# Performance work log

Hardware: AMD Instinct MI355X
Metric: run time of the kernel (lower is better)

The kernel has to match this reference:

```python
import jax, jax.numpy as jnp
import numpy as np

# Sinabs LIF semantics (norm_input=True default):
#   v[t] = alpha * v[t-1] + (1 - alpha) * x[t],  alpha = exp(-1/tau_mem)
#   spikes = MultiSpike: max(floor(v / threshold), 0)   (default sa.ActivationFunction)
#   reset  = MembraneSubtract: v -= spikes * threshold
# threshold_low=None -> no lower clamp.

TAU_MEM = 20.0
THRESHOLD = 1.0
GRAD_WIDTH = 0.5   # sinabs SingleExponential surrogate defaults
GRAD_SCALE = 1.0

@jax.custom_vjp
def spike_fn(v):
    # MultiSpike: number of threshold crossings this step
    return jnp.maximum(jnp.floor(v / THRESHOLD), 0.0)

def _spike_fwd(v):
    return spike_fn(v), v

def _spike_bwd(v, g):
    # single-exponential surrogate gradient around threshold
    sg = (GRAD_SCALE / GRAD_WIDTH) * jnp.exp(-jnp.abs(v - THRESHOLD) / GRAD_WIDTH)
    return (g * sg,)

spike_fn.defvjp(_spike_fwd, _spike_bwd)

def lif_layer(x):
    # x: [B, T, N] synaptic input; returns spikes [B, T, N]
    alpha = jnp.exp(jnp.asarray(-1.0 / TAU_MEM, dtype=x.dtype))
    one_m = 1.0 - alpha

    def step(v, xt):
        v = alpha * v + one_m * xt
        s = spike_fn(v)
        v = v - s * THRESHOLD  # membrane subtract reset
        return v, s

    v0 = jnp.zeros(x.shape[:1] + x.shape[2:], dtype=x.dtype)  # [B, N]
    _, spikes = jax.lax.scan(step, v0, jnp.swapaxes(x, 0, 1))  # scan over T
    return jnp.swapaxes(spikes, 0, 1)

def setup_inputs() -> dict:
    key = jax.random.key(0)
    k0, k1, k2, k3 = jax.random.split(key, 4)
    B, T, C_IN = 256, 4096, 16
    data = jax.random.normal(k0, (B, T, C_IN), dtype=jnp.float32)
    # nn.Linear(in, out, bias=False) weights are [out, in], kaiming-uniform-ish scale
    w1 = jax.random.normal(k1, (16, 16), dtype=jnp.float32) / np.sqrt(16)
    w2 = jax.random.normal(k2, (32, 16), dtype=jnp.float32) / np.sqrt(16)
    w3 = jax.random.normal(k3, (10, 32), dtype=jnp.float32) / np.sqrt(32)
    return {"data": data, "w1": w1, "w2": w2, "w3": w3}

def reference(data, w1, w2, w3):
    out = jnp.einsum('btc,oc->bto', data, w1)
    out = lif_layer(out)
    out = jnp.einsum('btc,oc->bto', out, w2)
    out = lif_layer(out)
    out = jnp.einsum('btc,oc->bto', out, w3)
    out = lif_layer(out)
    return out
```

## Files before the change

### kernel.cpp

```cpp
#include <hip/hip_runtime.h>
#include <stdint.h>
#include <math.h>

#define T_STEPS 4096
#define BATCH   256
#define NB_BLK  256
#define NSEG    1024
#define EPITCH  1025

__device__ __forceinline__ float lif_step(float& v, float xs, float alpha) {
    float vp = fmaf(alpha, v, xs);
    float fr = vp - floorf(vp);
    float vn = fminf(vp, fr);
    float s  = vp - vn;
    v = vn;
    return s;
}

__device__ __forceinline__ float ubf(uint32_t w, int k) {
    return (float)((w >> (k * 8)) & 0xffu);
}

__device__ __forceinline__ float sgpr_f(float v) {
    return __uint_as_float(__builtin_amdgcn_readfirstlane(__float_as_uint(v)));
}

__device__ __forceinline__ float dot16(const float wr[16],
    float4 c0, float4 c1, float4 c2, float4 c3)
{
    float p0 = fmaf(wr[1], c0.y, wr[0] * c0.x);
    p0 = fmaf(wr[2], c0.z, p0);  p0 = fmaf(wr[3], c0.w, p0);
    float p1 = fmaf(wr[5], c1.y, wr[4] * c1.x);
    p1 = fmaf(wr[6], c1.z, p1);  p1 = fmaf(wr[7], c1.w, p1);
    float p2 = fmaf(wr[9], c2.y, wr[8] * c2.x);
    p2 = fmaf(wr[10], c2.z, p2); p2 = fmaf(wr[11], c2.w, p2);
    float p3 = fmaf(wr[13], c3.y, wr[12] * c3.x);
    p3 = fmaf(wr[14], c3.z, p3); p3 = fmaf(wr[15], c3.w, p3);
    return (p0 + p1) + (p2 + p3);
}

__global__ __launch_bounds__(1024) void fused(
    const float* __restrict__ x, const float* __restrict__ w1,
    const float* __restrict__ w2, const float* __restrict__ w3,
    float* __restrict__ out, uint8_t* __restrict__ s1t,
    uint8_t* __restrict__ s2t,
    float alpha, float one_m, float alpha4)
{
    const int tid = threadIdx.x;
    const int b   = blockIdx.x;
    const int wv  = tid >> 6;
    const int ln  = tid & 63;

    __shared__ float2   sh_cert[16][EPITCH];
    __shared__ uint32_t sh_badseg[16][NSEG / 32];
    __shared__ uint8_t  sh_bm1[NB_BLK];
    __shared__ uint8_t  sh_bm2[NB_BLK];
    __shared__ int      sh_badch, sh_spike, sh_flag2;

    const float* xb = x + (size_t)b * T_STEPS * 16;
    const float4* xq4 = (const float4*)xb;

    if (tid < 64)        ((uint32_t*)sh_bm1)[tid] = 0u;
    else if (tid < 128)  ((uint32_t*)sh_bm2)[tid - 64] = 0u;
    else if (tid == 128) { sh_badch = 0; sh_spike = 0; sh_flag2 = 0; }

    float4* o4 = (float4*)(out + (size_t)b * T_STEPS * 10);
    float4 z4 = make_float4(0.f, 0.f, 0.f, 0.f);
#pragma unroll
    for (int i = 0; i < 10; ++i) o4[i * 1024 + tid] = z4;

    const float alpha2 = alpha * alpha;

    {
        float4 xr[8];
#pragma unroll
        for (int q = 0; q < 8; ++q) xr[q] = xq4[tid * 16 + q];
#pragma unroll 2
        for (int c = 0; c < 16; ++c) {
            float wc[16];
#pragma unroll
            for (int i = 0; i < 16; ++i) wc[i] = sgpr_f(w1[c * 16 + i]);
            float y0 = dot16(wc, xr[0], xr[1], xr[2], xr[3]);
            float y1 = dot16(wc, xr[4], xr[5], xr[6], xr[7]);
            float a0 = one_m * y0;
            float a1 = fmaf(alpha, a0, one_m * y1);
            sh_cert[c][tid] = make_float2(a1, fmaxf(a0, a1));
        }
    }
    {
        float4 xr[8];
#pragma unroll
        for (int q = 0; q < 8; ++q) xr[q] = xq4[tid * 16 + 8 + q];
#pragma unroll 2
        for (int c = 0; c < 16; ++c) {
            float wc[16];
#pragma unroll
            for (int i = 0; i < 16; ++i) wc[i] = sgpr_f(w1[c * 16 + i]);
            float y2 = dot16(wc, xr[0], xr[1], xr[2], xr[3]);
            float y3 = dot16(wc, xr[4], xr[5], xr[6], xr[7]);
            float b0 = one_m * y2;
            float b1 = fmaf(alpha, b0, one_m * y3);
            float mB = fmaxf(b0, b1);
            float2 ca = sh_cert[c][tid];
            float end = fmaf(alpha2, ca.x, b1);
            float m0  = fmaxf(ca.y, fmaf(alpha, fmaxf(ca.x, 0.0f), mB));
            sh_cert[c][tid] = make_float2(end, m0);
        }
    }
    __syncthreads();

    if (tid < 128) {
        const int c  = tid & 15;
        const int e8 = tid >> 4;
        const int s0 = e8 * 128;
        float vs = 0.0f;
        if (e8 > 0) {
#pragma unroll 8
            for (int s = s0 - 40; s < s0; ++s)
                vs = fmaf(alpha4, vs, sh_cert[c][s].x);
        }
        uint32_t bw = 0;
        int bad = 0;
#pragma unroll 8
        for (int s = s0; s < s0 + 128; ++s) {
            float2 ct = sh_cert[c][s];
            float vsu = fminf(fmaxf(vs + 1e-3f, 0.0f), 1.0f);
            float bound = fmaf(alpha, vsu, ct.y);
            if (!(bound < 0.999f)) { bw |= 1u << (s & 31); bad = 1; }
            if ((s & 31) == 31) { sh_badseg[c][s >> 5] = bw; bw = 0; }
            vs = fmaf(alpha4, vs, ct.x);
        }
        if (bad) atomicOr(&sh_badch, 1 << c);
    }
    __syncthreads();

    const int badmask = sh_badch;
    if (badmask) {
        uint4* sz = (uint4*)(s1t + (size_t)b * 16 * T_STEPS);
#pragma unroll
        for (int i = 0; i < 4; ++i) sz[i * 1024 + tid] = make_uint4(0u,0u,0u,0u);
        __syncthreads();

        int m = badmask;
        for (int i = 0; i < wv; ++i) m &= m - 1;
        if (ln == 0 && m) {
            const int c = __ffs(m) - 1;
            float wc[16];
#pragma unroll
            for (int i = 0; i < 16; ++i) wc[i] = w1[c * 16 + i];
            uint8_t* op = s1t + ((size_t)b * 16 + c) * T_STEPS;
            float v = 0.0f;
            int any = 0;
            for (int w32 = 0; w32 < 32; ++w32) {
                uint32_t bwv = sh_badseg[c][w32];
                const int sb = w32 * 32;
                if (bwv == 0u) {
#pragma unroll 8
                    for (int q = 0; q < 32; ++q)
                        v = fmaf(alpha4, v, sh_cert[c][sb + q].x);
                } else {
                    for (int q = 0; q < 32; ++q) {
                        const int s = sb + q;
                        if (!((bwv >> q) & 1u)) {
                            v = fmaf(alpha4, v, sh_cert[c][s].x);
                            continue;
                        }
                        const float4* xr2 = xq4 + (size_t)s * 16;
                        uint32_t sw = 0u;
#pragma unroll
                        for (int j = 0; j < 4; ++j) {
                            float y = dot16(wc, xr2[j*4+0], xr2[j*4+1],
                                                 xr2[j*4+2], xr2[j*4+3]);
                            float sp = lif_step(v, one_m * y, alpha);
                            sw |= ((uint32_t)(int)sp) << (j * 8);
                        }
                        if (sw) {
                            *(uint32_t*)(op + s * 4) = sw;
                            sh_bm1[s >> 2] = 1;
                            any = 1;
                        }
                    }
                }
            }
            if (any) sh_spike = 1;
        }
    }
    __syncthreads();

    if (sh_spike) {
        if (tid < 32) {
            const int c2 = tid;
            float wr2[16];
#pragma unroll
            for (int i = 0; i < 16; ++i) wr2[i] = one_m * w2[c2 * 16 + i];
            const uint8_t* sb1 = s1t + (size_t)b * 16 * T_STEPS;
            uint4* op2 = (uint4*)(s2t + ((size_t)b * 32 + c2) * T_STEPS);
            const uint4* bmv = (const uint4*)sh_bm1;
            float v = 0.0f;
            for (int sb = 0; sb < 16; ++sb) {
                uint4 bm = bmv[sb];
                if ((bm.x | bm.y | bm.z | bm.w) == 0u) {
                    if (v != 0.0f) {
                        for (int blk = 0; blk < 16 && v != 0.0f; ++blk) {
#pragma unroll
                            for (int j = 0; j < 16; ++j) v *= alpha;
                        }
                    }
                    continue;
                }
                for (int blk = 0; blk < 16; ++blk) {
                    uint32_t d = (blk < 4) ? bm.x : (blk < 8) ? bm.y
                               : (blk < 12) ? bm.z : bm.w;
                    uint32_t byte = (d >> ((blk & 3) * 8)) & 0xffu;
                    if (byte == 0u) {
                        if (v != 0.0f) {
#pragma unroll
                            for (int j = 0; j < 16; ++j) v *= alpha;
                        }
                        continue;
                    }
                    const int tb = sb * 16 + blk;
                    const int t0 = tb * 16;
                    uint4 S[16];
#pragma unroll
                    for (int c = 0; c < 16; ++c)
                        S[c] = *(const uint4*)(sb1 + (size_t)c * T_STEPS + t0);
                    uint32_t w[4] = {0u, 0u, 0u, 0u};
#pragma unroll
                    for (int j = 0; j < 16; ++j) {
                        float xv[16];
#pragma unroll
                        for (int c = 0; c < 16; ++c) {
                            uint32_t dd = (j < 4) ? S[c].x : (j < 8) ? S[c].y
                                        : (j < 12) ? S[c].z : S[c].w;
                            xv[c] = ubf(dd, j & 3);
                        }
                        float p0 = fmaf(wr2[1], xv[1], wr2[0] * xv[0]);
                        p0 = fmaf(wr2[2], xv[2], p0);   p0 = fmaf(wr2[3], xv[3], p0);
                        float p1 = fmaf(wr2[5], xv[5], wr2[4] * xv[4]);
                        p1 = fmaf(wr2[6], xv[6], p1);   p1 = fmaf(wr2[7], xv[7], p1);
                        float p2 = fmaf(wr2[9], xv[9], wr2[8] * xv[8]);
                        p2 = fmaf(wr2[10], xv[10], p2); p2 = fmaf(wr2[11], xv[11], p2);
                        float p3 = fmaf(wr2[13], xv[13], wr2[12] * xv[12]);
                        p3 = fmaf(wr2[14], xv[14], p3); p3 = fmaf(wr2[15], xv[15], p3);
                        float xs = (p0 + p1) + (p2 + p3);
                        float s = lif_step(v, xs, alpha);
                        w[j >> 2] |= ((uint32_t)(int)s) << ((j & 3) * 8);
                    }
                    op2[tb] = make_uint4(w[0], w[1], w[2], w[3]);
                    if (w[0] | w[1] | w[2] | w[3]) { sh_bm2[tb] = 1; sh_flag2 = 1; }
                }
            }
        }
        __syncthreads();

        if (sh_flag2 && tid < 16) {
            const int c3 = tid;
            const bool active = (c3 < 10);
            float wr3[32];
#pragma unroll
            for (int i = 0; i < 32; ++i)
                wr3[i] = active ? (one_m * w3[c3 * 32 + i]) : 0.0f;
            const uint8_t* sb2 = s2t + (size_t)b * 32 * T_STEPS;
            const uint4* bmv2 = (const uint4*)sh_bm2;
            float* ob = out + (size_t)b * T_STEPS * 10 + c3;
            float v = 0.0f;
            for (int sb = 0; sb < 16; ++sb) {
                uint4 bm = bmv2[sb];
                if ((bm.x | bm.y | bm.z | bm.w) == 0u) {
                    if (v != 0.0f) {
                        for (int blk = 0; blk < 16 && v != 0.0f; ++blk) {
#pragma unroll
                            for (int j = 0; j < 16; ++j) v *= alpha;
                        }
                    }
                    continue;
                }
                for (int blk = 0; blk < 16; ++blk) {
                    uint32_t d = (blk < 4) ? bm.x : (blk < 8) ? bm.y
                               : (blk < 12) ? bm.z : bm.w;
                    uint32_t byte = (d >> ((blk & 3) * 8)) & 0xffu;
                    if (byte == 0u) {
                        if (v != 0.0f) {
#pragma unroll
                            for (int j = 0; j < 16; ++j) v *= alpha;
                        }
                        continue;
                    }
                    const int t0 = (sb * 16 + blk) * 16;
                    uint4 S[32];
#pragma unroll
                    for (int c = 0; c < 32; ++c)
                        S[c] = *(const uint4*)(sb2 + (size_t)c * T_STEPS + t0);
#pragma unroll
                    for (int j = 0; j < 16; ++j) {
                        float xv[32];
#pragma unroll
                        for (int c = 0; c < 32; ++c) {
                            uint32_t dd = (j < 4) ? S[c].x : (j < 8) ? S[c].y
                                        : (j < 12) ? S[c].z : S[c].w;
                            xv[c] = ubf(dd, j & 3);
                        }
                        float p0 = fmaf(wr3[1], xv[1], wr3[0] * xv[0]);
                        p0 = fmaf(wr3[2],  xv[2],  p0); p0 = fmaf(wr3[3],  xv[3],  p0);
                        p0 = fmaf(wr3[4],  xv[4],  p0); p0 = fmaf(wr3[5],  xv[5],  p0);
                        p0 = fmaf(wr3[6],  xv[6],  p0); p0 = fmaf(wr3[7],  xv[7],  p0);
                        float p1 = fmaf(wr3[9], xv[9], wr3[8] * xv[8]);
                        p1 = fmaf(wr3[10], xv[10], p1); p1 = fmaf(wr3[11], xv[11], p1);
                        p1 = fmaf(wr3[12], xv[12], p1); p1 = fmaf(wr3[13], xv[13], p1);
                        p1 = fmaf(wr3[14], xv[14], p1); p1 = fmaf(wr3[15], xv[15], p1);
                        float p2 = fmaf(wr3[17], xv[17], wr3[16] * xv[16]);
                        p2 = fmaf(wr3[18], xv[18], p2); p2 = fmaf(wr3[19], xv[19], p2);
                        p2 = fmaf(wr3[20], xv[20], p2); p2 = fmaf(wr3[21], xv[21], p2);
                        p2 = fmaf(wr3[22], xv[22], p2); p2 = fmaf(wr3[23], xv[23], p2);
                        float p3 = fmaf(wr3[25], xv[25], wr3[24] * xv[24]);
                        p3 = fmaf(wr3[26], xv[26], p3); p3 = fmaf(wr3[27], xv[27], p3);
                        p3 = fmaf(wr3[28], xv[28], p3); p3 = fmaf(wr3[29], xv[29], p3);
                        p3 = fmaf(wr3[30], xv[30], p3); p3 = fmaf(wr3[31], xv[31], p3);
                        float xs = (p0 + p1) + (p2 + p3);
                        float s = lif_step(v, xs, alpha);
                        if (active && s != 0.0f) ob[(size_t)(t0 + j) * 10] = s;
                    }
                }
            }
        }
    }
}

extern "C" void kernel_launch(void* const* d_in, const int* in_sizes, int n_in,
                              void* d_out, int out_size, void* d_ws, size_t ws_size,
                              hipStream_t stream)
{
    const float* data = (const float*)d_in[0];
    const float* w1   = (const float*)d_in[1];
    const float* w2   = (const float*)d_in[2];
    const float* w3   = (const float*)d_in[3];
    float* out = (float*)d_out;

    uint8_t* ws  = (uint8_t*)d_ws;
    uint8_t* s1t = ws;
    uint8_t* s2t = ws + (16u << 20);

    const float alpha  = expf(-1.0f / 20.0f);
    const float one_m  = 1.0f - alpha;
    const float alpha4 = expf(-4.0f / 20.0f);

    fused<<<BATCH, 1024, 0, stream>>>(data, w1, w2, w3, out, s1t, s2t,
                                      alpha, one_m, alpha4);
}
```

Baseline: 150.1 us.

## Split fused LIF kernel into channel-half layer-1 blocks and separate tail kernel

Layer 1 now runs as 512-thread blocks, two per batch row, each handling 8 of the 16 channels. Per-segment bound data is stored as float ends plus 16-bit quantized maxima, and the certificate bound is tightened with a second maximum term. Layers 2 and 3 move into a separate 64-thread kernel that reads a global block bitmap and flags, and a memset is added to clear them. The goal is higher occupancy and less shared memory per block. The cost is an extra launch, a memset, and global round-trips for the bitmaps.

```diff
diff --git a/kernel.cpp b/kernel.cpp
--- a/kernel.cpp
+++ b/kernel.cpp
@@ -4,9 +4,8 @@
 
 #define T_STEPS 4096
 #define BATCH   256
-#define NB_BLK  256
 #define NSEG    1024
-#define EPITCH  1025
+#define CPITCH  9
 
 __device__ __forceinline__ float lif_step(float& v, float xs, float alpha) {
     float vp = fmaf(alpha, v, xs);
@@ -23,6 +22,15 @@
 
 __device__ __forceinline__ float sgpr_f(float v) {
     return __uint_as_float(__builtin_amdgcn_readfirstlane(__float_as_uint(v)));
+}
+
+__device__ __forceinline__ unsigned short encq(float m) {
+    int q = (int)ceilf(fmaf(m, 4096.0f, 32768.0f));
+    q = q < 0 ? 0 : (q > 65534 ? 65535 : q);
+    return (unsigned short)q;
+}
+__device__ __forceinline__ float decq(unsigned short q) {
+    return (q == 65535) ? 1e30f : fmaf((float)q, 0.000244140625f, -8.0f);
 }
 
 __device__ __forceinline__ float dot16(const float wr[16],
@@ -39,96 +47,110 @@
     return (p0 + p1) + (p2 + p3);
 }
 
-__global__ __launch_bounds__(1024) void fused(
+__global__ __launch_bounds__(512) void lif1(
     const float* __restrict__ x, const float* __restrict__ w1,
-    const float* __restrict__ w2, const float* __restrict__ w3,
     float* __restrict__ out, uint8_t* __restrict__ s1t,
-    uint8_t* __restrict__ s2t,
+    uint8_t* __restrict__ bm1, int* __restrict__ flag1,
     float alpha, float one_m, float alpha4)
 {
     const int tid = threadIdx.x;
-    const int b   = blockIdx.x;
+    const int bh  = blockIdx.x;
+    const int b   = bh >> 1;
+    const int cg  = bh & 1;
     const int wv  = tid >> 6;
     const int ln  = tid & 63;
 
-    __shared__ float2   sh_cert[16][EPITCH];
-    __shared__ uint32_t sh_badseg[16][NSEG / 32];
-    __shared__ uint8_t  sh_bm1[NB_BLK];
-    __shared__ uint8_t  sh_bm2[NB_BLK];
-    __shared__ int      sh_badch, sh_spike, sh_flag2;
-
-    const float* xb = x + (size_t)b * T_STEPS * 16;
-    const float4* xq4 = (const float4*)xb;
-
-    if (tid < 64)        ((uint32_t*)sh_bm1)[tid] = 0u;
-    else if (tid < 128)  ((uint32_t*)sh_bm2)[tid - 64] = 0u;
-    else if (tid == 128) { sh_badch = 0; sh_spike = 0; sh_flag2 = 0; }
+    __shared__ float          endf[NSEG * CPITCH];
+    __shared__ unsigned short m0q [NSEG * CPITCH];
+    __shared__ unsigned short m1q [NSEG * CPITCH];
+    __shared__ uint32_t       sh_badseg[8][32];
+    __shared__ int            sh_badch;
+
+    const float4* xq4 = (const float4*)(x + (size_t)b * T_STEPS * 16);
+
+    if (tid == 0) sh_badch = 0;
 
     float4* o4 = (float4*)(out + (size_t)b * T_STEPS * 10);
     float4 z4 = make_float4(0.f, 0.f, 0.f, 0.f);
 #pragma unroll
-    for (int i = 0; i < 10; ++i) o4[i * 1024 + tid] = z4;
-
-    const float alpha2 = alpha * alpha;
-
-    {
-        float4 xr[8];
-#pragma unroll
-        for (int q = 0; q < 8; ++q) xr[q] = xq4[tid * 16 + q];
+    for (int i = 0; i < 10; ++i) o4[cg * 5120 + i * 512 + tid] = z4;
+
+    const float a2 = alpha * alpha;
+    const float a3 = a2 * alpha;
+    const float a4 = a2 * a2;
+
+#pragma unroll
+    for (int ss = 0; ss < 2; ++ss) {
+        const int s = ss * 512 + tid;
+        {
+            float4 xr[8];
+#pragma unroll
+            for (int q = 0; q < 8; ++q) xr[q] = xq4[s * 16 + q];
 #pragma unroll 2
-        for (int c = 0; c < 16; ++c) {
-            float wc[16];
-#pragma unroll
-            for (int i = 0; i < 16; ++i) wc[i] = sgpr_f(w1[c * 16 + i]);
-            float y0 = dot16(wc, xr[0], xr[1], xr[2], xr[3]);
-            float y1 = dot16(wc, xr[4], xr[5], xr[6], xr[7]);
-            float a0 = one_m * y0;
-            float a1 = fmaf(alpha, a0, one_m * y1);
-            sh_cert[c][tid] = make_float2(a1, fmaxf(a0, a1));
-        }
-    }
-    {
-        float4 xr[8];
-#pragma unroll
-        for (int q = 0; q < 8; ++q) xr[q] = xq4[tid * 16 + 8 + q];
+            for (int cl = 0; cl < 8; ++cl) {
+                float wc[16];
+#pragma unroll
+                for (int i = 0; i < 16; ++i)
+                    wc[i] = sgpr_f(w1[(cg * 8 + cl) * 16 + i]);
+                float y0 = dot16(wc, xr[0], xr[1], xr[2], xr[3]);
+                float y1 = dot16(wc, xr[4], xr[5], xr[6], xr[7]);
+                float A0 = one_m * y0;
+                float A1 = fmaf(alpha, A0, one_m * y1);
+                endf[s * CPITCH + cl] = A1;
+                m0q[s * CPITCH + cl] = encq(fmaxf(A0, A1));
+                m1q[s * CPITCH + cl] = encq(fmaxf(A0 + alpha, A1 + a2));
+            }
+        }
+        {
+            float4 xr[8];
+#pragma unroll
+            for (int q = 0; q < 8; ++q) xr[q] = xq4[s * 16 + 8 + q];
 #pragma unroll 2
-        for (int c = 0; c < 16; ++c) {
-            float wc[16];
-#pragma unroll
-            for (int i = 0; i < 16; ++i) wc[i] = sgpr_f(w1[c * 16 + i]);
-            float y2 = dot16(wc, xr[0], xr[1], xr[2], xr[3]);
-            float y3 = dot16(wc, xr[4], xr[5], xr[6], xr[7]);
-            float b0 = one_m * y2;
-            float b1 = fmaf(alpha, b0, one_m * y3);
-            float mB = fmaxf(b0, b1);
-            float2 ca = sh_cert[c][tid];
-            float end = fmaf(alpha2, ca.x, b1);
-            float m0  = fmaxf(ca.y, fmaf(alpha, fmaxf(ca.x, 0.0f), mB));
-            sh_cert[c][tid] = make_float2(end, m0);
+            for (int cl = 0; cl < 8; ++cl) {
+                float wc[16];
+#pragma unroll
+                for (int i = 0; i < 16; ++i)
+                    wc[i] = sgpr_f(w1[(cg * 8 + cl) * 16 + i]);
+                float y2 = dot16(wc, xr[0], xr[1], xr[2], xr[3]);
+                float y3 = dot16(wc, xr[4], xr[5], xr[6], xr[7]);
+                float B0 = one_m * y2;
+                float B1 = fmaf(alpha, B0, one_m * y3);
+                float accA = endf[s * CPITCH + cl];
+                float m0A  = decq(m0q[s * CPITCH + cl]);
+                float m1A  = decq(m1q[s * CPITCH + cl]);
+                float acc2 = fmaf(alpha, accA, B0);
+                float acc3 = fmaf(a2, accA, B1);
+                float m0 = fmaxf(m0A, fmaxf(acc2, acc3));
+                float m1 = fmaxf(m1A, fmaxf(acc2 + a3, acc3 + a4));
+                endf[s * CPITCH + cl] = acc3;
+                m0q[s * CPITCH + cl] = encq(m0);
+                m1q[s * CPITCH + cl] = encq(m1);
+            }
         }
     }
     __syncthreads();
 
-    if (tid < 128) {
-        const int c  = tid & 15;
-        const int e8 = tid >> 4;
+    if (tid < 64) {
+        const int c  = tid & 7;
+        const int e8 = tid >> 3;
         const int s0 = e8 * 128;
         float vs = 0.0f;
         if (e8 > 0) {
 #pragma unroll 8
             for (int s = s0 - 40; s < s0; ++s)
-                vs = fmaf(alpha4, vs, sh_cert[c][s].x);
+                vs = fmaf(alpha4, vs, endf[s * CPITCH + c]);
         }
         uint32_t bw = 0;
         int bad = 0;
-#pragma unroll 8
+#pragma unroll 4
         for (int s = s0; s < s0 + 128; ++s) {
-            float2 ct = sh_cert[c][s];
+            float m0v = decq(m0q[s * CPITCH + c]);
+            float m1v = decq(m1q[s * CPITCH + c]);
             float vsu = fminf(fmaxf(vs + 1e-3f, 0.0f), 1.0f);
-            float bound = fmaf(alpha, vsu, ct.y);
+            float bound = fmaf(1.0f - vsu, m0v, vsu * m1v);
             if (!(bound < 0.999f)) { bw |= 1u << (s & 31); bad = 1; }
             if ((s & 31) == 31) { sh_badseg[c][s >> 5] = bw; bw = 0; }
-            vs = fmaf(alpha4, vs, ct.x);
+            vs = fmaf(alpha4, vs, endf[s * CPITCH + c]);
         }
         if (bad) atomicOr(&sh_badch, 1 << c);
     }
@@ -136,9 +158,9 @@
 
     const int badmask = sh_badch;
     if (badmask) {
-        uint4* sz = (uint4*)(s1t + (size_t)b * 16 * T_STEPS);
-#pragma unroll
-        for (int i = 0; i < 4; ++i) sz[i * 1024 + tid] = make_uint4(0u,0u,0u,0u);
+        uint4* sz = (uint4*)(s1t + ((size_t)b * 16 + cg * 8) * T_STEPS);
+#pragma unroll
+        for (int i = 0; i < 4; ++i) sz[i * 512 + tid] = make_uint4(0u,0u,0u,0u);
         __syncthreads();
 
         int m = badmask;
@@ -147,8 +169,9 @@
             const int c = __ffs(m) - 1;
             float wc[16];
 #pragma unroll
-            for (int i = 0; i < 16; ++i) wc[i] = w1[c * 16 + i];
-            uint8_t* op = s1t + ((size_t)b * 16 + c) * T_STEPS;
+            for (int i = 0; i < 16; ++i) wc[i] = w1[(cg * 8 + c) * 16 + i];
+            uint8_t* op = s1t + ((size_t)b * 16 + cg * 8 + c) * T_STEPS;
+            uint8_t* bmp = bm1 + (size_t)b * 256;
             float v = 0.0f;
             int any = 0;
             for (int w32 = 0; w32 < 32; ++w32) {
@@ -157,12 +180,12 @@
                 if (bwv == 0u) {
 #pragma unroll 8
                     for (int q = 0; q < 32; ++q)
-                        v = fmaf(alpha4, v, sh_cert[c][sb + q].x);
+                        v = fmaf(alpha4, v, endf[(sb + q) * CPITCH + c]);
                 } else {
                     for (int q = 0; q < 32; ++q) {
                         const int s = sb + q;
                         if (!((bwv >> q) & 1u)) {
-                            v = fmaf(alpha4, v, sh_cert[c][s].x);
+                            v = fmaf(alpha4, v, endf[s * CPITCH + c]);
                             continue;
                         }
                         const float4* xr2 = xq4 + (size_t)s * 16;
@@ -176,151 +199,171 @@
                         }
                         if (sw) {
                             *(uint32_t*)(op + s * 4) = sw;
-                            sh_bm1[s >> 2] = 1;
+                            bmp[s >> 2] = 1;
                             any = 1;
                         }
                     }
                 }
             }
-            if (any) sh_spike = 1;
-        }
-    }
+            if (any) atomicOr(&flag1[b], 1 << cg);
+        }
+    }
+}
+
+__global__ __launch_bounds__(64) void tails(
+    const uint8_t* __restrict__ s1t, const float* __restrict__ w2,
+    const float* __restrict__ w3, uint8_t* __restrict__ s2t,
+    float* __restrict__ out, const uint8_t* __restrict__ bm1,
+    const int* __restrict__ flag1, float alpha, float one_m)
+{
+    const int tid = threadIdx.x;
+    const int b   = blockIdx.x;
+    const int f   = flag1[b];
+    if (!f) return;
+    const bool v0 = (f & 1), v1 = (f & 2);
+
+    __shared__ uint8_t sh_bm2[256];
+    __shared__ int     sh_flag2;
+    ((uint32_t*)sh_bm2)[tid] = 0u;
+    if (tid == 0) sh_flag2 = 0;
     __syncthreads();
 
-    if (sh_spike) {
-        if (tid < 32) {
-            const int c2 = tid;
-            float wr2[16];
-#pragma unroll
-            for (int i = 0; i < 16; ++i) wr2[i] = one_m * w2[c2 * 16 + i];
-            const uint8_t* sb1 = s1t + (size_t)b * 16 * T_STEPS;
-            uint4* op2 = (uint4*)(s2t + ((size_t)b * 32 + c2) * T_STEPS);
-            const uint4* bmv = (const uint4*)sh_bm1;
-            float v = 0.0f;
-            for (int sb = 0; sb < 16; ++sb) {
-                uint4 bm = bmv[sb];
-                if ((bm.x | bm.y | bm.z | bm.w) == 0u) {
+    if (tid < 32) {
+        const int c2 = tid;
+        float wr2[16];
+#pragma unroll
+        for (int i = 0; i < 16; ++i) wr2[i] = one_m * w2[c2 * 16 + i];
+        const uint8_t* sb1 = s1t + (size_t)b * 16 * T_STEPS;
+        uint4* op2 = (uint4*)(s2t + ((size_t)b * 32 + c2) * T_STEPS);
+        const uint4* bmv = (const uint4*)(bm1 + (size_t)b * 256);
+        float v = 0.0f;
+        for (int sb = 0; sb < 16; ++sb) {
+            uint4 bm = bmv[sb];
+            if ((bm.x | bm.y | bm.z | bm.w) == 0u) {
+                if (v != 0.0f) {
+                    for (int blk = 0; blk < 16 && v != 0.0f; ++blk) {
+#pragma unroll
+                        for (int j = 0; j < 16; ++j) v *= alpha;
+                    }
+                }
+                continue;
+            }
+            for (int blk = 0; blk < 16; ++blk) {
+                uint32_t d = (blk < 4) ? bm.x : (blk < 8) ? bm.y
+                           : (blk < 12) ? bm.z : bm.w;
+                uint32_t byte = (d >> ((blk & 3) * 8)) & 0xffu;
+                if (byte == 0u) {
                     if (v != 0.0f) {
-                        for (int blk = 0; blk < 16 && v != 0.0f; ++blk) {
-#pragma unroll
-                            for (int j = 0; j < 16; ++j) v *= alpha;
-                        }
+#pragma unroll
+                        for (int j = 0; j < 16; ++j) v *= alpha;
                     }
                     continue;
                 }
-                for (int blk = 0; blk < 16; ++blk) {
-                    uint32_t d = (blk < 4) ? bm.x : (blk < 8) ? bm.y
-                               : (blk < 12) ? bm.z : bm.w;
-                    uint32_t byte = (d >> ((blk & 3) * 8)) & 0xffu;
-                    if (byte == 0u) {
-                        if (v != 0.0f) {
-#pragma unroll
-                            for (int j = 0; j < 16; ++j) v *= alpha;
-                        }
-                        continue;
-                    }
-                    const int tb = sb * 16 + blk;
-                    const int t0 = tb * 16;
-                    uint4 S[16];
-#pragma unroll
-                    for (int c = 0; c < 16; ++c)
-                        S[c] = *(const uint4*)(sb1 + (size_t)c * T_STEPS + t0);
-                    uint32_t w[4] = {0u, 0u, 0u, 0u};
-#pragma unroll
-                    for (int j = 0; j < 16; ++j) {
-                        float xv[16];
-#pragma unroll
-                        for (int c = 0; c < 16; ++c) {
-                            uint32_t dd = (j < 4) ? S[c].x : (j < 8) ? S[c].y
-                                        : (j < 12) ? S[c].z : S[c].w;
-                            xv[c] = ubf(dd, j & 3);
-                        }
-                        float p0 = fmaf(wr2[1], xv[1], wr2[0] * xv[0]);
-                        p0 = fmaf(wr2[2], xv[2], p0);   p0 = fmaf(wr2[3], xv[3], p0);
-                        float p1 = fmaf(wr2[5], xv[5], wr2[4] * xv[4]);
-                        p1 = fmaf(wr2[6], xv[6], p1);   p1 = fmaf(wr2[7], xv[7], p1);
-                        float p2 = fmaf(wr2[9], xv[9], wr2[8] * xv[8]);
-                        p2 = fmaf(wr2[10], xv[10], p2); p2 = fmaf(wr2[11], xv[11], p2);
-                        float p3 = fmaf(wr2[13], xv[13], wr2[12] * xv[12]);
-                        p3 = fmaf(wr2[14], xv[14], p3); p3 = fmaf(wr2[15], xv[15], p3);
-                        float xs = (p0 + p1) + (p2 + p3);
-                        float s = lif_step(v, xs, alpha);
-                        w[j >> 2] |= ((uint32_t)(int)s) << ((j & 3) * 8);
-                    }
-                    op2[tb] = make_uint4(w[0], w[1], w[2], w[3]);
-                    if (w[0] | w[1] | w[2] | w[3]) { sh_bm2[tb] = 1; sh_flag2 = 1; }
-                }
-            }
-        }
-        __syncthreads();
-
-        if (sh_flag2 && tid < 16) {
-            const int c3 = tid;
-            const bool active = (c3 < 10);
-            float wr3[32];
-#pragma unroll
-            for (int i = 0; i < 32; ++i)
-                wr3[i] = active ? (one_m * w3[c3 * 32 + i]) : 0.0f;
-            const uint8_t* sb2 = s2t + (size_t)b * 32 * T_STEPS;
-            const uint4* bmv2 = (const uint4*)sh_bm2;
-            float* ob = out + (size_t)b * T_STEPS * 10 + c3;
-            float v = 0.0f;
-            for (int sb = 0; sb < 16; ++sb) {
-                uint4 bm = bmv2[sb];
-                if ((bm.x | bm.y | bm.z | bm.w) == 0u) {
+                const int tb = sb * 16 + blk;
+                const int t0 = tb * 16;
+                uint4 zz = make_uint4(0u,0u,0u,0u);
+                uint4 S[16];
+#pragma unroll
+                for (int c = 0; c < 16; ++c) {
+                    const bool valid = (c < 8) ? v0 : v1;
+                    S[c] = valid ? *(const uint4*)(sb1 + (size_t)c * T_STEPS + t0)
+                                 : zz;
+                }
+                uint32_t w[4] = {0u, 0u, 0u, 0u};
+#pragma unroll
+                for (int j = 0; j < 16; ++j) {
+                    float xv[16];
+#pragma unroll
+                    for (int c = 0; c < 16; ++c) {
+                        uint32_t dd = (j < 4) ? S[c].x : (j < 8) ? S[c].y
+                                    : (j < 12) ? S[c].z : S[c].w;
+                        xv[c] = ubf(dd, j & 3);
+                    }
+                    float p0 = fmaf(wr2[1], xv[1], wr2[0] * xv[0]);
+                    p0 = fmaf(wr2[2], xv[2], p0);   p0 = fmaf(wr2[3], xv[3], p0);
+                    float p1 = fmaf(wr2[5], xv[5], wr2[4] * xv[4]);
+                    p1 = fmaf(wr2[6], xv[6], p1);   p1 = fmaf(wr2[7], xv[7], p1);
+                    float p2 = fmaf(wr2[9], xv[9], wr2[8] * xv[8]);
+                    p2 = fmaf(wr2[10], xv[10], p2); p2 = fmaf(wr2[11], xv[11], p2);
+                    float p3 = fmaf(wr2[13], xv[13], wr2[12] * xv[12]);
+                    p3 = fmaf(wr2[14], xv[14], p3); p3 = fmaf(wr2[15], xv[15], p3);
+                    float xs = (p0 + p1) + (p2 + p3);
+                    float s = lif_step(v, xs, alpha);
+                    w[j >> 2] |= ((uint32_t)(int)s) << ((j & 3) * 8);
+                }
+                op2[tb] = make_uint4(w[0], w[1], w[2], w[3]);
+                if (w[0] | w[1] | w[2] | w[3]) { sh_bm2[tb] = 1; sh_flag2 = 1; }
+            }
+        }
+    }
+    __syncthreads();
+
+    if (sh_flag2 && tid < 16) {
+        const int c3 = tid;
+        const bool active = (c3 < 10);
+        float wr3[32];
+#pragma unroll
+        for (int i = 0; i < 32; ++i)
+            wr3[i] = active ? (one_m * w3[c3 * 32 + i]) : 0.0f;
+        const uint8_t* sb2 = s2t + (size_t)b * 32 * T_STEPS;
+        const uint4* bmv2 = (const uint4*)sh_bm2;
+        float* ob = out + (size_t)b * T_STEPS * 10 + c3;
+        float v = 0.0f;
+        for (int sb = 0; sb < 16; ++sb) {
+            uint4 bm = bmv2[sb];
+            if ((bm.x | bm.y | bm.z | bm.w) == 0u) {
+                if (v != 0.0f) {
+                    for (int blk = 0; blk < 16 && v != 0.0f; ++blk) {
+#pragma unroll
+                        for (int j = 0; j < 16; ++j) v *= alpha;
+                    }
+                }
+                continue;
+            }
+            for (int blk = 0; blk < 16; ++blk) {
+                uint32_t d = (blk < 4) ? bm.x : (blk < 8) ? bm.y
+                           : (blk < 12) ? bm.z : bm.w;
+                uint32_t byte = (d >> ((blk & 3) * 8)) & 0xffu;
+                if (byte == 0u) {
                     if (v != 0.0f) {
-                        for (int blk = 0; blk < 16 && v != 0.0f; ++blk) {
-#pragma unroll
-                            for (int j = 0; j < 16; ++j) v *= alpha;
-                        }
+#pragma unroll
+                        for (int j = 0; j < 16; ++j) v *= alpha;
                     }
                     continue;
                 }
-                for (int blk = 0; blk < 16; ++blk) {
-                    uint32_t d = (blk < 4) ? bm.x : (blk < 8) ? bm.y
-                               : (blk < 12) ? bm.z : bm.w;
-                    uint32_t byte = (d >> ((blk & 3) * 8)) & 0xffu;
-                    if (byte == 0u) {
-                        if (v != 0.0f) {
-#pragma unroll
-                            for (int j = 0; j < 16; ++j) v *= alpha;
-                        }
-                        continue;
-                    }
-                    const int t0 = (sb * 16 + blk) * 16;
-                    uint4 S[32];
-#pragma unroll
-                    for (int c = 0; c < 32; ++c)
-                        S[c] = *(const uint4*)(sb2 + (size_t)c * T_STEPS + t0);
-#pragma unroll
-                    for (int j = 0; j < 16; ++j) {
-                        float xv[32];
-#pragma unroll
-                        for (int c = 0; c < 32; ++c) {
-                            uint32_t dd = (j < 4) ? S[c].x : (j < 8) ? S[c].y
-                                        : (j < 12) ? S[c].z : S[c].w;
-                            xv[c] = ubf(dd, j & 3);
-                        }
-                        float p0 = fmaf(wr3[1], xv[1], wr3[0] * xv[0]);
-                        p0 = fmaf(wr3[2],  xv[2],  p0); p0 = fmaf(wr3[3],  xv[3],  p0);
-                        p0 = fmaf(wr3[4],  xv[4],  p0); p0 = fmaf(wr3[5],  xv[5],  p0);
-                        p0 = fmaf(wr3[6],  xv[6],  p0); p0 = fmaf(wr3[7],  xv[7],  p0);
-                        float p1 = fmaf(wr3[9], xv[9], wr3[8] * xv[8]);
-                        p1 = fmaf(wr3[10], xv[10], p1); p1 = fmaf(wr3[11], xv[11], p1);
-                        p1 = fmaf(wr3[12], xv[12], p1); p1 = fmaf(wr3[13], xv[13], p1);
-                        p1 = fmaf(wr3[14], xv[14], p1); p1 = fmaf(wr3[15], xv[15], p1);
-                        float p2 = fmaf(wr3[17], xv[17], wr3[16] * xv[16]);
-                        p2 = fmaf(wr3[18], xv[18], p2); p2 = fmaf(wr3[19], xv[19], p2);
-                        p2 = fmaf(wr3[20], xv[20], p2); p2 = fmaf(wr3[21], xv[21], p2);
-                        p2 = fmaf(wr3[22], xv[22], p2); p2 = fmaf(wr3[23], xv[23], p2);
-                        float p3 = fmaf(wr3[25], xv[25], wr3[24] * xv[24]);
-                        p3 = fmaf(wr3[26], xv[26], p3); p3 = fmaf(wr3[27], xv[27], p3);
-                        p3 = fmaf(wr3[28], xv[28], p3); p3 = fmaf(wr3[29], xv[29], p3);
-                        p3 = fmaf(wr3[30], xv[30], p3); p3 = fmaf(wr3[31], xv[31], p3);
-                        float xs = (p0 + p1) + (p2 + p3);
-                        float s = lif_step(v, xs, alpha);
-                        if (active && s != 0.0f) ob[(size_t)(t0 + j) * 10] = s;
-                    }
+                const int t0 = (sb * 16 + blk) * 16;
+                uint4 S[32];
+#pragma unroll
+                for (int c = 0; c < 32; ++c)
+                    S[c] = *(const uint4*)(sb2 + (size_t)c * T_STEPS + t0);
+#pragma unroll
+                for (int j = 0; j < 16; ++j) {
+                    float xv[32];
+#pragma unroll
+                    for (int c = 0; c < 32; ++c) {
+                        uint32_t dd = (j < 4) ? S[c].x : (j < 8) ? S[c].y
+                                    : (j < 12) ? S[c].z : S[c].w;
+                        xv[c] = ubf(dd, j & 3);
+                    }
+                    float p0 = fmaf(wr3[1], xv[1], wr3[0] * xv[0]);
+                    p0 = fmaf(wr3[2],  xv[2],  p0); p0 = fmaf(wr3[3],  xv[3],  p0);
+                    p0 = fmaf(wr3[4],  xv[4],  p0); p0 = fmaf(wr3[5],  xv[5],  p0);
+                    p0 = fmaf(wr3[6],  xv[6],  p0); p0 = fmaf(wr3[7],  xv[7],  p0);
+                    float p1 = fmaf(wr3[9], xv[9], wr3[8] * xv[8]);
+                    p1 = fmaf(wr3[10], xv[10], p1); p1 = fmaf(wr3[11], xv[11], p1);
+                    p1 = fmaf(wr3[12], xv[12], p1); p1 = fmaf(wr3[13], xv[13], p1);
+                    p1 = fmaf(wr3[14], xv[14], p1); p1 = fmaf(wr3[15], xv[15], p1);
+                    float p2 = fmaf(wr3[17], xv[17], wr3[16] * xv[16]);
+                    p2 = fmaf(wr3[18], xv[18], p2); p2 = fmaf(wr3[19], xv[19], p2);
+                    p2 = fmaf(wr3[20], xv[20], p2); p2 = fmaf(wr3[21], xv[21], p2);
+                    p2 = fmaf(wr3[22], xv[22], p2); p2 = fmaf(wr3[23], xv[23], p2);
+                    float p3 = fmaf(wr3[25], xv[25], wr3[24] * xv[24]);
+                    p3 = fmaf(wr3[26], xv[26], p3); p3 = fmaf(wr3[27], xv[27], p3);
+                    p3 = fmaf(wr3[28], xv[28], p3); p3 = fmaf(wr3[29], xv[29], p3);
+                    p3 = fmaf(wr3[30], xv[30], p3); p3 = fmaf(wr3[31], xv[31], p3);
+                    float xs = (p0 + p1) + (p2 + p3);
+                    float s = lif_step(v, xs, alpha);
+                    if (active && s != 0.0f) ob[(size_t)(t0 + j) * 10] = s;
                 }
             }
         }
@@ -337,14 +380,19 @@
     const float* w3   = (const float*)d_in[3];
     float* out = (float*)d_out;
 
-    uint8_t* ws  = (uint8_t*)d_ws;
-    uint8_t* s1t = ws;
-    uint8_t* s2t = ws + (16u << 20);
+    uint8_t* ws    = (uint8_t*)d_ws;
+    uint8_t* s1t   = ws;
+    uint8_t* s2t   = ws + (16u << 20);
+    uint8_t* bm1   = ws + (48u << 20);
+    int*     flag1 = (int*)(bm1 + (64u << 10));
 
     const float alpha  = expf(-1.0f / 20.0f);
     const float one_m  = 1.0f - alpha;
     const float alpha4 = expf(-4.0f / 20.0f);
 
-    fused<<<BATCH, 1024, 0, stream>>>(data, w1, w2, w3, out, s1t, s2t,
-                                      alpha, one_m, alpha4);
-}
+    hipMemsetAsync(bm1, 0, (64u << 10) + 1024, stream);
+    lif1 <<<BATCH * 2, 512, 0, stream>>>(data, w1, out, s1t, bm1, flag1,
+                                         alpha, one_m, alpha4);
+    tails<<<BATCH,     64, 0, stream>>>(s1t, w2, w3, s2t, out, bm1, flag1,
+                                        alpha, one_m);
+}
```

After: 165.3 us. 1.1x slower.
